# Performance work log

Measured on AMD Instinct MI355X. Metric: run time of the kernel, lower is better.

Reference implementation:

```python
import jax, jax.numpy as jnp
import numpy as np

EPS = 1e-5

def setup_inputs() -> dict:
    key = jax.random.key(0)
    k1, k2, k3 = jax.random.split(key, 3)
    B, P, N, Cin, Cout = 16384, 32, 2, 9, 64
    pillars = jax.random.normal(k1, (B, P, N, Cin), dtype=jnp.float32)
    num_points_per_pillar = jax.random.randint(k2, (B, P), 0, N, dtype=jnp.int32)
    # nn.Linear(9, 64, bias=False): weight (out, in), kaiming-uniform-ish init
    W = jax.random.normal(k3, (Cout, Cin), dtype=jnp.float32) * (1.0 / np.sqrt(Cin))
    gamma = jnp.ones((Cout,), dtype=jnp.float32)
    beta = jnp.zeros((Cout,), dtype=jnp.float32)
    return {"pillars": pillars, "num_points_per_pillar": num_points_per_pillar,
            "W": W, "gamma": gamma, "beta": beta}

def reference(pillars, num_points_per_pillar, W, gamma, beta):
    # pillars: (B, P, N, Cin) -> linear (no bias) -> (B, P, N, Cout)
    B, P, N, _ = pillars.shape
    x = jnp.einsum('bpnc,oc->bpno', pillars, W)
    # permute(0,3,1,2): (B, Cout, P, N)
    x = jnp.transpose(x, (0, 3, 1, 2))
    C = x.shape[1]
    # BatchNorm1d(64) applied to (B*C, P*N); requires P*N == 64.
    # Training mode: batch stats over dim 0, biased variance.
    x2 = x.reshape(B * C, P * N)
    mean = jnp.mean(x2, axis=0)            # (P*N,) == (64,)
    var = jnp.mean(jnp.square(x2 - mean), axis=0)
    x2 = (x2 - mean) * jax.lax.rsqrt(var + EPS) * gamma + beta
    x = jax.nn.relu(x2).reshape(B, C, P, N)
    # max over the point dim N -> (B, C, P)
    return jnp.max(x, axis=3)
```

## Files before the change

### kernel.cpp

```cpp
#include <hip/hip_runtime.h>


#define EPS_BN 1e-5f

__global__ __launch_bounds__(64) void pfn_prep(const float* __restrict__ W,
                                               float* __restrict__ ws) {
    __shared__ float prod[64][90];
    const int o = threadIdx.x;
    float w[9];
#pragma unroll
    for (int c = 0; c < 9; ++c) w[c] = W[o * 9 + c];
#pragma unroll
    for (int c = 0; c < 9; ++c)
#pragma unroll
        for (int c2 = 0; c2 < 9; ++c2) prod[o][c * 9 + c2] = w[c] * w[c2];
#pragma unroll
    for (int c = 0; c < 9; ++c) prod[o][81 + c] = w[c];
#pragma unroll
    for (int k = 0; k < 16; ++k) ws[96 + o * 16 + k] = 0.f;
    __syncthreads();
    for (int col = o; col < 90; col += 64) {
        float s = 0.f;
        for (int r = 0; r < 64; ++r) s += prod[r][col];
        ws[col] = s;
    }
}

__global__ __launch_bounds__(256) void pfn_stats(const float* __restrict__ pillars,
                                                 const float* __restrict__ gw,
                                                 float* __restrict__ acc8) {
    __shared__ float smG[96];
    __shared__ float red[4][32][5];

    const int tid = threadIdx.x;
    const int wv = tid >> 6;
    const int lane = tid & 63;
    const int p = lane & 31;
    const int bsub = lane >> 5;

    if (tid < 90) smG[tid] = gw[tid];
    __syncthreads();

    float d0 = 0.f, d1 = 0.f, q0 = 0.f, q1 = 0.f;
#pragma unroll
    for (int it = 0; it < 2; ++it) {
        const int pr = blockIdx.x * 4 + wv + it * 4096;
        const int b = pr * 2 + bsub;
        const float2* src = (const float2*)(pillars + (size_t)b * 576 + p * 18);
        float v[18];
#pragma unroll
        for (int k = 0; k < 9; ++k) {
            const float2 t = src[k];
            v[2 * k] = t.x;
            v[2 * k + 1] = t.y;
        }
#pragma unroll
        for (int c = 0; c < 9; ++c) {
            const float wc = smG[81 + c];
            d0 = fmaf(wc, v[c], d0);
            d1 = fmaf(wc, v[9 + c], d1);
            float t0 = 0.f, t1 = 0.f;
#pragma unroll
            for (int c2 = 0; c2 < 9; ++c2) {
                const float g = smG[c * 9 + c2];
                t0 = fmaf(g, v[c2], t0);
                t1 = fmaf(g, v[9 + c2], t1);
            }
            q0 = fmaf(v[c], t0, q0);
            q1 = fmaf(v[9 + c], t1, q1);
        }
    }
    d0 += __shfl_xor(d0, 32); q0 += __shfl_xor(q0, 32);
    d1 += __shfl_xor(d1, 32); q1 += __shfl_xor(q1, 32);
    if (lane < 32) {
        red[wv][p][0] = d0; red[wv][p][1] = q0;
        red[wv][p][2] = d1; red[wv][p][3] = q1;
    }
    __syncthreads();
    if (tid < 32) {
        float s0 = 0.f, s1 = 0.f, s2 = 0.f, s3 = 0.f;
#pragma unroll
        for (int w = 0; w < 4; ++w) {
            s0 += red[w][tid][0]; s1 += red[w][tid][1];
            s2 += red[w][tid][2]; s3 += red[w][tid][3];
        }
        float* acc = acc8 + (blockIdx.x & 7) * 128;
        atomicAdd(&acc[(2 * tid) * 2], s0);
        atomicAdd(&acc[(2 * tid) * 2 + 1], s1);
        atomicAdd(&acc[(2 * tid + 1) * 2], s2);
        atomicAdd(&acc[(2 * tid + 1) * 2 + 1], s3);
    }
}

__global__ __launch_bounds__(256) void pfn_main(const float* __restrict__ pillars,
                                                const float* __restrict__ W,
                                                const float* __restrict__ acc8,
                                                const float* __restrict__ gamma,
                                                const float* __restrict__ beta,
                                                float* __restrict__ out,
                                                float invBC) {
    __shared__ float smW[64 * 12];
    __shared__ float smAB[128];

    const int tid = threadIdx.x;
    for (int i = tid; i < 576; i += 256) smW[(i / 9) * 12 + (i % 9)] = W[i];
    if (tid < 64) {
        float s1 = 0.f, s2 = 0.f;
#pragma unroll
        for (int s = 0; s < 8; ++s) {
            s1 += acc8[s * 128 + tid * 2];
            s2 += acc8[s * 128 + tid * 2 + 1];
        }
        const float mean = s1 * invBC;
        const float var = s2 * invBC - mean * mean;
        const float a = rsqrtf(var + EPS_BN) * gamma[tid];
        smAB[tid] = a;
        smAB[64 + tid] = beta[tid] - mean * a;
    }
    __syncthreads();

    const int g = tid >> 5;
    const int p = tid & 31;
    float wr[72];
#pragma unroll
    for (int k = 0; k < 8; ++k) {
        const int o = g * 8 + k;
        const float4 wa = *(const float4*)&smW[o * 12];
        const float4 wb = *(const float4*)&smW[o * 12 + 4];
        wr[k * 9 + 0] = wa.x; wr[k * 9 + 1] = wa.y;
        wr[k * 9 + 2] = wa.z; wr[k * 9 + 3] = wa.w;
        wr[k * 9 + 4] = wb.x; wr[k * 9 + 5] = wb.y;
        wr[k * 9 + 6] = wb.z; wr[k * 9 + 7] = wb.w;
        wr[k * 9 + 8] = smW[o * 12 + 8];
    }
    const float a0 = smAB[2 * p], a1 = smAB[2 * p + 1];
    const float bb0 = smAB[64 + 2 * p], bb1 = smAB[64 + 2 * p + 1];

    const float* Pb0 = pillars + (size_t)blockIdx.x * 8 * 576 + p * 18;
    float* Ob0 = out + (size_t)blockIdx.x * 16384 + g * 256 + p;
#pragma unroll 2
    for (int bl = 0; bl < 8; ++bl) {
        float vs0[9], vs1[9];
        {
            const float2* src = (const float2*)(Pb0 + bl * 576);
#pragma unroll
            for (int k = 0; k < 4; ++k) {
                const float2 t = src[k];
                vs0[2 * k] = t.x * a0;
                vs0[2 * k + 1] = t.y * a0;
            }
            {
                const float2 t = src[4];
                vs0[8] = t.x * a0;
                vs1[0] = t.y * a1;
            }
#pragma unroll
            for (int k = 0; k < 4; ++k) {
                const float2 t = src[5 + k];
                vs1[1 + 2 * k] = t.x * a1;
                vs1[2 + 2 * k] = t.y * a1;
            }
        }
        float* Ob = Ob0 + bl * 2048;
#pragma unroll
        for (int k = 0; k < 8; ++k) {
            float x0 = bb0, x1 = bb1;
#pragma unroll
            for (int c = 0; c < 9; ++c) {
                x0 = fmaf(wr[k * 9 + c], vs0[c], x0);
                x1 = fmaf(wr[k * 9 + c], vs1[c], x1);
            }
            Ob[k * 32] = fmaxf(fmaxf(x0, x1), 0.f);
        }
    }
}

extern "C" void kernel_launch(void* const* d_in, const int* in_sizes, int n_in,
                              void* d_out, int out_size, void* d_ws, size_t ws_size,
                              hipStream_t stream) {
    const float* pillars = (const float*)d_in[0];
    const float* W = (const float*)d_in[2];
    const float* gamma = (const float*)d_in[3];
    const float* beta = (const float*)d_in[4];
    float* out = (float*)d_out;
    float* ws = (float*)d_ws;

    const int B = in_sizes[0] / 576;
    const float invBC = 1.0f / ((float)B * 64.0f);

    pfn_prep<<<1, 64, 0, stream>>>(W, ws);
    pfn_stats<<<B / 16, 256, 0, stream>>>(pillars, ws, ws + 96);
    pfn_main<<<B / 8, 256, 0, stream>>>(pillars, W, ws + 96, gamma, beta, out,
                                        invBC);
}
```

Measured before the change: 192.5 us.

## Stage pillars through LDS with coalesced float4 loads and drop prep kernel

Both the stats and main kernels now load pillar data with fully coalesced float4 global reads into shared memory, transposed to channel-major layout, instead of strided per-thread float2 reads. The Gram-matrix precompute moves into each stats block, and the separate prep kernel is replaced by a memset of the accumulators. This targets poor coalescing of the 72-byte-strided loads, at the cost of extra LDS traffic, integer div/mod index math, redundant per-block Gram computation and more shared memory per block, which may lower occupancy.

```diff
diff --git a/kernel.cpp b/kernel.cpp
--- a/kernel.cpp
+++ b/kernel.cpp
@@ -3,92 +3,88 @@
 
 #define EPS_BN 1e-5f
 
-__global__ __launch_bounds__(64) void pfn_prep(const float* __restrict__ W,
-                                               float* __restrict__ ws) {
-    __shared__ float prod[64][90];
-    const int o = threadIdx.x;
-    float w[9];
-#pragma unroll
-    for (int c = 0; c < 9; ++c) w[c] = W[o * 9 + c];
-#pragma unroll
-    for (int c = 0; c < 9; ++c)
-#pragma unroll
-        for (int c2 = 0; c2 < 9; ++c2) prod[o][c * 9 + c2] = w[c] * w[c2];
-#pragma unroll
-    for (int c = 0; c < 9; ++c) prod[o][81 + c] = w[c];
-#pragma unroll
-    for (int k = 0; k < 16; ++k) ws[96 + o * 16 + k] = 0.f;
-    __syncthreads();
-    for (int col = o; col < 90; col += 64) {
-        float s = 0.f;
-        for (int r = 0; r < 64; ++r) s += prod[r][col];
-        ws[col] = s;
-    }
-}
-
 __global__ __launch_bounds__(256) void pfn_stats(const float* __restrict__ pillars,
-                                                 const float* __restrict__ gw,
+                                                 const float* __restrict__ W,
                                                  float* __restrict__ acc8) {
+    __shared__ float smS[5760];
     __shared__ float smG[96];
-    __shared__ float red[4][32][5];
+    __shared__ float red[4][64][2];
 
     const int tid = threadIdx.x;
     const int wv = tid >> 6;
     const int lane = tid & 63;
-    const int p = lane & 31;
-    const int bsub = lane >> 5;
+    const float4* P4 = (const float4*)pillars;
 
-    if (tid < 90) smG[tid] = gw[tid];
+    if (tid < 64) {
+        float w[9];
+#pragma unroll
+        for (int c = 0; c < 9; ++c) w[c] = W[tid * 9 + c];
+        float* row = &smS[tid * 90];
+#pragma unroll
+        for (int c = 0; c < 9; ++c)
+#pragma unroll
+            for (int c2 = 0; c2 < 9; ++c2) row[c * 9 + c2] = w[c] * w[c2];
+#pragma unroll
+        for (int c = 0; c < 9; ++c) row[81 + c] = w[c];
+    }
     __syncthreads();
+    if (tid < 90) {
+        float s = 0.f;
+        for (int r = 0; r < 64; ++r) s += smS[r * 90 + tid];
+        smG[tid] = s;
+    }
 
-    float d0 = 0.f, d1 = 0.f, q0 = 0.f, q1 = 0.f;
+    float dacc = 0.f, qacc = 0.f;
+    for (int pass = 0; pass < 2; ++pass) {
+        __syncthreads();
+        const int base4 = (blockIdx.x * 16 + pass * 8) * 144;
+        for (int i = tid; i < 1152; i += 256) {
+            const float4 g4 = P4[base4 + i];
+            const float comp[4] = {g4.x, g4.y, g4.z, g4.w};
+            const int f0 = 4 * i;
 #pragma unroll
-    for (int it = 0; it < 2; ++it) {
-        const int pr = blockIdx.x * 4 + wv + it * 4096;
-        const int b = pr * 2 + bsub;
-        const float2* src = (const float2*)(pillars + (size_t)b * 576 + p * 18);
-        float v[18];
+            for (int t = 0; t < 4; ++t) {
+                const int ff = f0 + t;
+                const int bl = ff / 576;
+                const int r = ff - bl * 576;
+                const int j = r / 9;
+                const int c = r - j * 9;
+                smS[bl * 576 + c * 64 + j] = comp[t];
+            }
+        }
+        __syncthreads();
 #pragma unroll
-        for (int k = 0; k < 9; ++k) {
-            const float2 t = src[k];
-            v[2 * k] = t.x;
-            v[2 * k + 1] = t.y;
-        }
+        for (int bb = 0; bb < 2; ++bb) {
+            const float* src = &smS[(wv * 2 + bb) * 576];
+            float v[9];
 #pragma unroll
-        for (int c = 0; c < 9; ++c) {
-            const float wc = smG[81 + c];
-            d0 = fmaf(wc, v[c], d0);
-            d1 = fmaf(wc, v[9 + c], d1);
-            float t0 = 0.f, t1 = 0.f;
+            for (int c = 0; c < 9; ++c) v[c] = src[c * 64 + lane];
+            float d = 0.f, q = 0.f;
 #pragma unroll
-            for (int c2 = 0; c2 < 9; ++c2) {
-                const float g = smG[c * 9 + c2];
-                t0 = fmaf(g, v[c2], t0);
-                t1 = fmaf(g, v[9 + c2], t1);
+            for (int c = 0; c < 9; ++c) {
+                d = fmaf(smG[81 + c], v[c], d);
+                float t = 0.f;
+#pragma unroll
+                for (int c2 = 0; c2 < 9; ++c2) t = fmaf(smG[c * 9 + c2], v[c2], t);
+                q = fmaf(v[c], t, q);
             }
-            q0 = fmaf(v[c], t0, q0);
-            q1 = fmaf(v[9 + c], t1, q1);
+            dacc += d;
+            qacc += q;
         }
     }
-    d0 += __shfl_xor(d0, 32); q0 += __shfl_xor(q0, 32);
-    d1 += __shfl_xor(d1, 32); q1 += __shfl_xor(q1, 32);
-    if (lane < 32) {
-        red[wv][p][0] = d0; red[wv][p][1] = q0;
-        red[wv][p][2] = d1; red[wv][p][3] = q1;
-    }
+    red[wv][lane][0] = dacc;
+    red[wv][lane][1] = qacc;
     __syncthreads();
-    if (tid < 32) {
-        float s0 = 0.f, s1 = 0.f, s2 = 0.f, s3 = 0.f;
+    if (tid < 64) {
+        float sd = 0.f, sq = 0.f;
 #pragma unroll
         for (int w = 0; w < 4; ++w) {
-            s0 += red[w][tid][0]; s1 += red[w][tid][1];
-            s2 += red[w][tid][2]; s3 += red[w][tid][3];
+            sd += red[w][tid][0];
+            sq += red[w][tid][1];
         }
         float* acc = acc8 + (blockIdx.x & 7) * 128;
-        atomicAdd(&acc[(2 * tid) * 2], s0);
-        atomicAdd(&acc[(2 * tid) * 2 + 1], s1);
-        atomicAdd(&acc[(2 * tid + 1) * 2], s2);
-        atomicAdd(&acc[(2 * tid + 1) * 2 + 1], s3);
+        atomicAdd(&acc[tid * 2], sd);
+        atomicAdd(&acc[tid * 2 + 1], sq);
     }
 }
 
@@ -99,10 +95,30 @@
                                                 const float* __restrict__ beta,
                                                 float* __restrict__ out,
                                                 float invBC) {
+    __shared__ float smT[8 * 576];
     __shared__ float smW[64 * 12];
     __shared__ float smAB[128];
 
     const int tid = threadIdx.x;
+    const float4* P4 = (const float4*)pillars;
+
+    {
+        const int base4 = blockIdx.x * 1152;
+        for (int i = tid; i < 1152; i += 256) {
+            const float4 g4 = P4[base4 + i];
+            const float comp[4] = {g4.x, g4.y, g4.z, g4.w};
+            const int f0 = 4 * i;
+#pragma unroll
+            for (int t = 0; t < 4; ++t) {
+                const int ff = f0 + t;
+                const int bl = ff / 576;
+                const int r = ff - bl * 576;
+                const int j = r / 9;
+                const int c = r - j * 9;
+                smT[bl * 576 + c * 64 + j] = comp[t];
+            }
+        }
+    }
     for (int i = tid; i < 576; i += 256) smW[(i / 9) * 12 + (i % 9)] = W[i];
     if (tid < 64) {
         float s1 = 0.f, s2 = 0.f;
@@ -136,29 +152,17 @@
     const float a0 = smAB[2 * p], a1 = smAB[2 * p + 1];
     const float bb0 = smAB[64 + 2 * p], bb1 = smAB[64 + 2 * p + 1];
 
-    const float* Pb0 = pillars + (size_t)blockIdx.x * 8 * 576 + p * 18;
     float* Ob0 = out + (size_t)blockIdx.x * 16384 + g * 256 + p;
 #pragma unroll 2
     for (int bl = 0; bl < 8; ++bl) {
         float vs0[9], vs1[9];
         {
-            const float2* src = (const float2*)(Pb0 + bl * 576);
+            const float* src = &smT[bl * 576];
 #pragma unroll
-            for (int k = 0; k < 4; ++k) {
-                const float2 t = src[k];
-                vs0[2 * k] = t.x * a0;
-                vs0[2 * k + 1] = t.y * a0;
-            }
-            {
-                const float2 t = src[4];
-                vs0[8] = t.x * a0;
-                vs1[0] = t.y * a1;
-            }
-#pragma unroll
-            for (int k = 0; k < 4; ++k) {
-                const float2 t = src[5 + k];
-                vs1[1 + 2 * k] = t.x * a1;
-                vs1[2 + 2 * k] = t.y * a1;
+            for (int c = 0; c < 9; ++c) {
+                const float2 t = *(const float2*)&src[c * 64 + 2 * p];
+                vs0[c] = t.x * a0;
+                vs1[c] = t.y * a1;
             }
         }
         float* Ob = Ob0 + bl * 2048;
@@ -188,8 +192,7 @@
     const int B = in_sizes[0] / 576;
     const float invBC = 1.0f / ((float)B * 64.0f);
 
-    pfn_prep<<<1, 64, 0, stream>>>(W, ws);
-    pfn_stats<<<B / 16, 256, 0, stream>>>(pillars, ws, ws + 96);
-    pfn_main<<<B / 8, 256, 0, stream>>>(pillars, W, ws + 96, gamma, beta, out,
-                                        invBC);
+    hipMemsetAsync(ws, 0, 1024 * sizeof(float), stream);
+    pfn_stats<<<B / 16, 256, 0, stream>>>(pillars, W, ws);
+    pfn_main<<<B / 8, 256, 0, stream>>>(pillars, W, ws, gamma, beta, out, invBC);
 }
```

Result: no change. 189.7 us (-1.4%).
